# Kernel tuning notes

Measured on AMD Instinct MI355X. Metric: run time of the kernel, lower is better.

The kernel has to match this reference:

```python
import jax, jax.numpy as jnp
import numpy as np

N_MELS, HIDDEN, HEAD_DIM = 80, 128, 64


def _gru_step(h, gx_t, w_hh, b_hh):
    # PyTorch GRU cell math. gx_t = x_t @ W_ih^T + b_ih, precomputed. [B, 3H]
    H = h.shape[-1]
    gh = h @ w_hh.T + b_hh  # [B, 3H]
    r = jax.nn.sigmoid(gx_t[:, :H] + gh[:, :H])
    z = jax.nn.sigmoid(gx_t[:, H:2 * H] + gh[:, H:2 * H])
    n = jnp.tanh(gx_t[:, 2 * H:] + r * gh[:, 2 * H:])
    return (1.0 - z) * n + z * h


def setup_inputs() -> dict:
    key = jax.random.key(0)
    ks = jax.random.split(key, 14)
    s = 1.0 / np.sqrt(HIDDEN)
    u = lambda k, shape, sc: jax.random.uniform(k, shape, jnp.float32, -sc, sc)
    return {
        "x": jax.random.normal(ks[0], (128, 1500, N_MELS), dtype=jnp.float32),
        # forward-direction GRU params
        "w_ih_f": u(ks[1], (3 * HIDDEN, N_MELS), s),
        "w_hh_f": u(ks[2], (3 * HIDDEN, HIDDEN), s),
        "b_ih_f": u(ks[3], (3 * HIDDEN,), s),
        "b_hh_f": u(ks[4], (3 * HIDDEN,), s),
        # backward-direction GRU params
        "w_ih_b": u(ks[5], (3 * HIDDEN, N_MELS), s),
        "w_hh_b": u(ks[6], (3 * HIDDEN, HIDDEN), s),
        "b_ih_b": u(ks[7], (3 * HIDDEN,), s),
        "b_hh_b": u(ks[8], (3 * HIDDEN,), s),
        # MLP head: Linear(2H, 64) -> ReLU -> Linear(64, 1)
        "w1": u(ks[9], (HEAD_DIM, 2 * HIDDEN), 1.0 / np.sqrt(2 * HIDDEN)),
        "b1": u(ks[10], (HEAD_DIM,), 1.0 / np.sqrt(2 * HIDDEN)),
        "w2": u(ks[11], (1, HEAD_DIM), 1.0 / np.sqrt(HEAD_DIM)),
        "b2": u(ks[12], (1,), 1.0 / np.sqrt(HEAD_DIM)),
    }


def reference(x, w_ih_f, w_hh_f, b_ih_f, b_hh_f, w_ih_b, w_hh_b, b_ih_b, b_hh_b, w1, b1, w2, b2):
    B, T, _ = x.shape
    h0 = jnp.zeros((B, HIDDEN), dtype=x.dtype)

    # Forward direction: last output = final hidden state after full scan.
    # Precompute input projections for all timesteps in one GEMM.
    gx_f = jnp.einsum('bti,gi->tbg', x, w_ih_f) + b_ih_f  # [T, B, 3H]
    h_f, _ = jax.lax.scan(lambda h, g: (_gru_step(h, g, w_hh_f, b_hh_f), None), h0, gx_f)

    # Backward direction: out[:, -1, H:] in PyTorch is the backward hidden
    # after processing ONLY x[:, -1] (the reverse scan's first step), so a
    # single GRU step from h0 reproduces it exactly.
    gx_b_last = x[:, -1, :] @ w_ih_b.T + b_ih_b  # [B, 3H]
    h_b = _gru_step(h0, gx_b_last, w_hh_b, b_hh_b)

    last = jnp.concatenate([h_f, h_b], axis=-1)  # [B, 2H]
    # Head (eval mode: dropout is identity)
    hdn = jax.nn.relu(last @ w1.T + b1)
    out = hdn @ w2.T + b2  # [B, 1]
    return out[:, 0]
```

## Files before the change

### kernel.cpp

```cpp
#include <hip/hip_runtime.h>

#define B 128
#define T 1500
#define NI 80
#define H 128
#define G 384
#define TT 64

typedef float v2f __attribute__((ext_vector_type(2)));

__device__ __forceinline__ float sigf(float x) { return 1.0f / (1.0f + __expf(-x)); }
__device__ __forceinline__ float tanhfast(float x) { return 1.0f - 2.0f / (1.0f + __expf(2.0f * x)); }
__device__ __forceinline__ v2f pkfma(v2f a, v2f b, v2f c) { return __builtin_elementwise_fma(a, b, c); }

__global__ __launch_bounds__(384)
void gx_gemm_kernel(const float* __restrict__ x, const float* __restrict__ w_ih,
                    const float* __restrict__ b_ih, float* __restrict__ gx,
                    int t0, int ct) {
    int tile = blockIdx.x;
    int b = blockIdx.y;
    int tl0 = tile * TT;
    if (tl0 >= ct) return;
    int n = (ct - tl0 < TT) ? (ct - tl0) : TT;
    int tid = threadIdx.x;

    __shared__ __align__(16) float xs[TT * NI];
    const float4* xsrc4 = (const float4*)(x + ((size_t)b * T + (size_t)(t0 + tl0)) * NI);
    int total4 = n * (NI / 4);
    for (int i = tid; i < total4; i += 384) ((float4*)xs)[i] = xsrc4[i];

    v2f w2[40];
    const v2f* wr = (const v2f*)(w_ih + (size_t)tid * NI);
#pragma unroll
    for (int i = 0; i < 40; ++i) w2[i] = wr[i];
    float bias = b_ih[tid];
    __syncthreads();

    float* gout = gx + ((size_t)b * ct + (size_t)tl0) * G + tid;
    int tt = 0;
    for (; tt + 2 <= n; tt += 2) {
        const float4* xa4 = (const float4*)(xs + tt * NI);
        const float4* xb4 = (const float4*)(xs + (tt + 1) * NI);
        v2f a0 = {0.f, 0.f}, a1 = {0.f, 0.f}, c0 = {0.f, 0.f}, c1 = {0.f, 0.f};
#pragma unroll
        for (int i = 0; i < 20; ++i) {
            float4 xa = xa4[i];
            float4 xb = xb4[i];
            v2f alo = {xa.x, xa.y}, ahi = {xa.z, xa.w};
            v2f blo = {xb.x, xb.y}, bhi = {xb.z, xb.w};
            a0 = pkfma(w2[2 * i], alo, a0);
            a1 = pkfma(w2[2 * i + 1], ahi, a1);
            c0 = pkfma(w2[2 * i], blo, c0);
            c1 = pkfma(w2[2 * i + 1], bhi, c1);
        }
        gout[(size_t)tt * G]       = bias + ((a0.x + a0.y) + (a1.x + a1.y));
        gout[(size_t)(tt + 1) * G] = bias + ((c0.x + c0.y) + (c1.x + c1.y));
    }
    if (tt < n) {
        const float4* xa4 = (const float4*)(xs + tt * NI);
        v2f a0 = {0.f, 0.f}, a1 = {0.f, 0.f};
#pragma unroll
        for (int i = 0; i < 20; ++i) {
            float4 xa = xa4[i];
            v2f alo = {xa.x, xa.y}, ahi = {xa.z, xa.w};
            a0 = pkfma(w2[2 * i], alo, a0);
            a1 = pkfma(w2[2 * i + 1], ahi, a1);
        }
        gout[(size_t)tt * G] = bias + ((a0.x + a0.y) + (a1.x + a1.y));
    }
}

__global__ __launch_bounds__(512)
void scan_kernel(const float* __restrict__ gx, const float* __restrict__ w_hh,
                 const float* __restrict__ b_hh, float* __restrict__ h_state,
                 int ct, int first, int last,
                 const float* __restrict__ x,
                 const float* __restrict__ w_ih_b, const float* __restrict__ b_ih_b,
                 const float* __restrict__ b_hh_b,
                 const float* __restrict__ w1, const float* __restrict__ b1,
                 const float* __restrict__ w2, const float* __restrict__ b2,
                 float* __restrict__ out) {
    int b = blockIdx.x;
    int tid = threadIdx.x;
    int j = tid >> 2;
    int q = tid & 3;
    int jpad = j + ((j >> 5) << 2);

    __shared__ __align__(16) float hs0[144];
    __shared__ __align__(16) float hs1[144];
    __shared__ __align__(16) float tail_gx[G];
    __shared__ __align__(16) float last_s[2 * H];
    __shared__ __align__(16) float xb_s[NI];

    v2f WR[16], WZ[16], WN[16];
    {
        const v2f* p0 = (const v2f*)(w_hh + (size_t)j * H + 32 * q);
        const v2f* p1 = (const v2f*)(w_hh + (size_t)(j + H) * H + 32 * q);
        const v2f* p2 = (const v2f*)(w_hh + (size_t)(j + 2 * H) * H + 32 * q);
#pragma unroll
        for (int i = 0; i < 16; ++i) { WR[i] = p0[i]; WZ[i] = p1[i]; WN[i] = p2[i]; }
    }
    float br = b_hh[j], bz = b_hh[j + H], bn = b_hh[j + 2 * H];

    float h_cur = 0.f;
    if (!first) h_cur = h_state[b * H + j];
    if (q == 0) hs0[jpad] = h_cur;

    float ga0, ga1, ga2, gb0 = 0.f, gb1 = 0.f, gb2 = 0.f;
    {
        const float* gp = gx + (size_t)b * ct * G;
        ga0 = gp[j]; ga1 = gp[j + H]; ga2 = gp[j + 2 * H];
        if (ct > 1) { gb0 = gp[G + j]; gb1 = gp[G + j + H]; gb2 = gp[G + j + 2 * H]; }
    }
    asm volatile("s_waitcnt lgkmcnt(0)\n\ts_barrier" ::: "memory");

    auto step = [&](int TL, const float* SRC, float* DST, float& g0, float& g1, float& g2) {
        const float4* hv4 = (const float4*)(SRC + 36 * q);
        v2f arv = {0.f, 0.f}, azv = {0.f, 0.f}, anv = {0.f, 0.f};
#pragma unroll
        for (int i = 0; i < 8; ++i) {
            float4 hv = hv4[i];
            v2f hlo = {hv.x, hv.y}, hhi = {hv.z, hv.w};
            arv = pkfma(WR[2 * i], hlo, arv);
            azv = pkfma(WZ[2 * i], hlo, azv);
            anv = pkfma(WN[2 * i], hlo, anv);
            arv = pkfma(WR[2 * i + 1], hhi, arv);
            azv = pkfma(WZ[2 * i + 1], hhi, azv);
            anv = pkfma(WN[2 * i + 1], hhi, anv);
        }
        float ar = arv.x + arv.y, az = azv.x + azv.y, an = anv.x + anv.y;
        ar += __shfl_xor(ar, 1); az += __shfl_xor(az, 1); an += __shfl_xor(an, 1);
        ar += __shfl_xor(ar, 2); az += __shfl_xor(az, 2); an += __shfl_xor(an, 2);
        float r = sigf(g0 + br + ar);
        float z = sigf(g1 + bz + az);
        float n = tanhfast(g2 + r * (bn + an));
        h_cur = (1.f - z) * n + z * h_cur;
        if (q == 0) DST[jpad] = h_cur;
        if (TL + 2 < ct) {
            const float* gp = gx + ((size_t)b * ct + TL + 2) * G;
            g0 = gp[j]; g1 = gp[j + H]; g2 = gp[j + 2 * H];
        }
        asm volatile("s_waitcnt lgkmcnt(0)\n\ts_barrier" ::: "memory");
    };

    int tl = 0;
    for (; tl + 1 < ct; tl += 2) {
        step(tl,     hs0, hs1, ga0, ga1, ga2);
        step(tl + 1, hs1, hs0, gb0, gb1, gb2);
    }
    if (tl < ct) step(tl, hs0, hs1, ga0, ga1, ga2);

    if (!last) {
        if (q == 0) h_state[b * H + j] = h_cur;
        return;
    }

    if (tid < NI) xb_s[tid] = x[((size_t)b * T + (T - 1)) * NI + tid];
    if (q == 0) last_s[j] = h_cur;
    __syncthreads();

    if (tid < G) {
        const float4* wbr = (const float4*)(w_ih_b + (size_t)tid * NI);
        const float4* xv = (const float4*)xb_s;
        float a0 = 0.f, a1 = 0.f, a2 = 0.f, a3 = 0.f;
#pragma unroll
        for (int i = 0; i < 20; ++i) {
            float4 wv = wbr[i]; float4 x4 = xv[i];
            a0 = fmaf(wv.x, x4.x, a0); a1 = fmaf(wv.y, x4.y, a1);
            a2 = fmaf(wv.z, x4.z, a2); a3 = fmaf(wv.w, x4.w, a3);
        }
        tail_gx[tid] = b_ih_b[tid] + ((a0 + a1) + (a2 + a3));
    }
    __syncthreads();

    if (tid < H) {
        float r = sigf(tail_gx[tid] + b_hh_b[tid]);
        float z = sigf(tail_gx[tid + H] + b_hh_b[tid + H]);
        float n = tanhfast(tail_gx[tid + 2 * H] + r * b_hh_b[tid + 2 * H]);
        last_s[H + tid] = (1.f - z) * n;
    }
    __syncthreads();

    if (tid < 64) {
        const float4* w1r = (const float4*)(w1 + (size_t)tid * 2 * H);
        const float4* lv = (const float4*)last_s;
        float a0 = 0.f, a1 = 0.f, a2 = 0.f, a3 = 0.f;
#pragma unroll
        for (int i = 0; i < 64; ++i) {
            float4 wv = w1r[i]; float4 l4 = lv[i];
            a0 = fmaf(wv.x, l4.x, a0); a1 = fmaf(wv.y, l4.y, a1);
            a2 = fmaf(wv.z, l4.z, a2); a3 = fmaf(wv.w, l4.w, a3);
        }
        float v = b1[tid] + ((a0 + a1) + (a2 + a3));
        v = fmaxf(v, 0.f) * w2[tid];
#pragma unroll
        for (int off = 32; off > 0; off >>= 1) v += __shfl_down(v, off);
        if (tid == 0) out[b] = v + b2[0];
    }
}

extern "C" void kernel_launch(void* const* d_in, const int* in_sizes, int n_in,
                              void* d_out, int out_size, void* d_ws, size_t ws_size,
                              hipStream_t stream) {
    (void)in_sizes; (void)n_in; (void)out_size;
    const float* x      = (const float*)d_in[0];
    const float* w_ih_f = (const float*)d_in[1];
    const float* w_hh_f = (const float*)d_in[2];
    const float* b_ih_f = (const float*)d_in[3];
    const float* b_hh_f = (const float*)d_in[4];
    const float* w_ih_b = (const float*)d_in[5];
    const float* w_hh_b = (const float*)d_in[6];
    const float* b_ih_b = (const float*)d_in[7];
    const float* b_hh_b = (const float*)d_in[8];
    const float* w1     = (const float*)d_in[9];
    const float* b1     = (const float*)d_in[10];
    const float* w2     = (const float*)d_in[11];
    const float* b2     = (const float*)d_in[12];
    (void)w_hh_b;
    float* out = (float*)d_out;

    float* h_state = (float*)d_ws;
    float* gxbuf = h_state + B * H;
    size_t hbytes = (size_t)B * H * sizeof(float);
    size_t avail = ws_size > hbytes ? ws_size - hbytes : 0;
    long long chunkT = (long long)(avail / ((size_t)B * G * sizeof(float)));
    if (chunkT > T) chunkT = T;
    if (chunkT < 1) chunkT = 1;

    for (int t0 = 0; t0 < T; t0 += (int)chunkT) {
        int ct = (T - t0 < (int)chunkT) ? (T - t0) : (int)chunkT;
        int ntiles = (ct + TT - 1) / TT;
        gx_gemm_kernel<<<dim3(ntiles, B), dim3(384), 0, stream>>>(
            x, w_ih_f, b_ih_f, gxbuf, t0, ct);
        scan_kernel<<<dim3(B), dim3(512), 0, stream>>>(
            gxbuf, w_hh_f, b_hh_f, h_state, ct,
            (t0 == 0) ? 1 : 0, (t0 + ct >= T) ? 1 : 0,
            x, w_ih_b, b_ih_b, b_hh_b, w1, b1, w2, b2, out);
    }
}
```

Measured before the change: 1.163 ms.

## Fuse input projection into the GRU scan kernel, dropping the gx buffer

```diff
diff --git a/kernel.cpp b/kernel.cpp
--- a/kernel.cpp
+++ b/kernel.cpp
@@ -5,7 +5,6 @@
 #define NI 80
 #define H 128
 #define G 384
-#define TT 64
 
 typedef float v2f __attribute__((ext_vector_type(2)));
 
@@ -13,73 +12,15 @@
 __device__ __forceinline__ float tanhfast(float x) { return 1.0f - 2.0f / (1.0f + __expf(2.0f * x)); }
 __device__ __forceinline__ v2f pkfma(v2f a, v2f b, v2f c) { return __builtin_elementwise_fma(a, b, c); }
 
-__global__ __launch_bounds__(384)
-void gx_gemm_kernel(const float* __restrict__ x, const float* __restrict__ w_ih,
-                    const float* __restrict__ b_ih, float* __restrict__ gx,
-                    int t0, int ct) {
-    int tile = blockIdx.x;
-    int b = blockIdx.y;
-    int tl0 = tile * TT;
-    if (tl0 >= ct) return;
-    int n = (ct - tl0 < TT) ? (ct - tl0) : TT;
-    int tid = threadIdx.x;
-
-    __shared__ __align__(16) float xs[TT * NI];
-    const float4* xsrc4 = (const float4*)(x + ((size_t)b * T + (size_t)(t0 + tl0)) * NI);
-    int total4 = n * (NI / 4);
-    for (int i = tid; i < total4; i += 384) ((float4*)xs)[i] = xsrc4[i];
-
-    v2f w2[40];
-    const v2f* wr = (const v2f*)(w_ih + (size_t)tid * NI);
-#pragma unroll
-    for (int i = 0; i < 40; ++i) w2[i] = wr[i];
-    float bias = b_ih[tid];
-    __syncthreads();
-
-    float* gout = gx + ((size_t)b * ct + (size_t)tl0) * G + tid;
-    int tt = 0;
-    for (; tt + 2 <= n; tt += 2) {
-        const float4* xa4 = (const float4*)(xs + tt * NI);
-        const float4* xb4 = (const float4*)(xs + (tt + 1) * NI);
-        v2f a0 = {0.f, 0.f}, a1 = {0.f, 0.f}, c0 = {0.f, 0.f}, c1 = {0.f, 0.f};
-#pragma unroll
-        for (int i = 0; i < 20; ++i) {
-            float4 xa = xa4[i];
-            float4 xb = xb4[i];
-            v2f alo = {xa.x, xa.y}, ahi = {xa.z, xa.w};
-            v2f blo = {xb.x, xb.y}, bhi = {xb.z, xb.w};
-            a0 = pkfma(w2[2 * i], alo, a0);
-            a1 = pkfma(w2[2 * i + 1], ahi, a1);
-            c0 = pkfma(w2[2 * i], blo, c0);
-            c1 = pkfma(w2[2 * i + 1], bhi, c1);
-        }
-        gout[(size_t)tt * G]       = bias + ((a0.x + a0.y) + (a1.x + a1.y));
-        gout[(size_t)(tt + 1) * G] = bias + ((c0.x + c0.y) + (c1.x + c1.y));
-    }
-    if (tt < n) {
-        const float4* xa4 = (const float4*)(xs + tt * NI);
-        v2f a0 = {0.f, 0.f}, a1 = {0.f, 0.f};
-#pragma unroll
-        for (int i = 0; i < 20; ++i) {
-            float4 xa = xa4[i];
-            v2f alo = {xa.x, xa.y}, ahi = {xa.z, xa.w};
-            a0 = pkfma(w2[2 * i], alo, a0);
-            a1 = pkfma(w2[2 * i + 1], ahi, a1);
-        }
-        gout[(size_t)tt * G] = bias + ((a0.x + a0.y) + (a1.x + a1.y));
-    }
-}
-
 __global__ __launch_bounds__(512)
-void scan_kernel(const float* __restrict__ gx, const float* __restrict__ w_hh,
-                 const float* __restrict__ b_hh, float* __restrict__ h_state,
-                 int ct, int first, int last,
-                 const float* __restrict__ x,
-                 const float* __restrict__ w_ih_b, const float* __restrict__ b_ih_b,
-                 const float* __restrict__ b_hh_b,
-                 const float* __restrict__ w1, const float* __restrict__ b1,
-                 const float* __restrict__ w2, const float* __restrict__ b2,
-                 float* __restrict__ out) {
+void fused_gru_kernel(const float* __restrict__ x,
+                      const float* __restrict__ w_ih, const float* __restrict__ b_ih,
+                      const float* __restrict__ w_hh, const float* __restrict__ b_hh,
+                      const float* __restrict__ w_ih_b, const float* __restrict__ b_ih_b,
+                      const float* __restrict__ b_hh_b,
+                      const float* __restrict__ w1, const float* __restrict__ b1,
+                      const float* __restrict__ w2, const float* __restrict__ b2,
+                      float* __restrict__ out) {
     int b = blockIdx.x;
     int tid = threadIdx.x;
     int j = tid >> 2;
@@ -100,59 +41,80 @@
 #pragma unroll
         for (int i = 0; i < 16; ++i) { WR[i] = p0[i]; WZ[i] = p1[i]; WN[i] = p2[i]; }
     }
-    float br = b_hh[j], bz = b_hh[j + H], bn = b_hh[j + 2 * H];
+    float4 XWR[5], XWZ[5], XWN[5];
+    {
+        const float4* p0 = (const float4*)(w_ih + (size_t)j * NI + 20 * q);
+        const float4* p1 = (const float4*)(w_ih + (size_t)(j + H) * NI + 20 * q);
+        const float4* p2 = (const float4*)(w_ih + (size_t)(j + 2 * H) * NI + 20 * q);
+#pragma unroll
+        for (int i = 0; i < 5; ++i) { XWR[i] = p0[i]; XWZ[i] = p1[i]; XWN[i] = p2[i]; }
+    }
+    float brz = b_hh[j] ;
+    float bzz = b_hh[j + H];
+    float bnh = b_hh[j + 2 * H];
+    float cr = b_ih[j] + brz;
+    float cz = b_ih[j + H] + bzz;
+    float cn = b_ih[j + 2 * H];
+
+    const float* xbase = x + (size_t)b * T * NI + 20 * q;
+    float4 XA[5], XB[5];
+#pragma unroll
+    for (int i = 0; i < 5; ++i) XA[i] = *(const float4*)(xbase + i * 4);
+#pragma unroll
+    for (int i = 0; i < 5; ++i) XB[i] = *(const float4*)(xbase + NI + i * 4);
 
     float h_cur = 0.f;
-    if (!first) h_cur = h_state[b * H + j];
-    if (q == 0) hs0[jpad] = h_cur;
+    if (q == 0) hs0[jpad] = 0.f;
+    __syncthreads();
 
-    float ga0, ga1, ga2, gb0 = 0.f, gb1 = 0.f, gb2 = 0.f;
-    {
-        const float* gp = gx + (size_t)b * ct * G;
-        ga0 = gp[j]; ga1 = gp[j + H]; ga2 = gp[j + 2 * H];
-        if (ct > 1) { gb0 = gp[G + j]; gb1 = gp[G + j + H]; gb2 = gp[G + j + 2 * H]; }
-    }
-    asm volatile("s_waitcnt lgkmcnt(0)\n\ts_barrier" ::: "memory");
-
-    auto step = [&](int TL, const float* SRC, float* DST, float& g0, float& g1, float& g2) {
+    auto step = [&](int TL, const float* SRC, float* DST, float4 (&XC)[5]) {
         const float4* hv4 = (const float4*)(SRC + 36 * q);
-        v2f arv = {0.f, 0.f}, azv = {0.f, 0.f}, anv = {0.f, 0.f};
+        v2f arv = {0.f, 0.f}, azv = {0.f, 0.f}, anh = {0.f, 0.f}, anx = {0.f, 0.f};
 #pragma unroll
         for (int i = 0; i < 8; ++i) {
             float4 hv = hv4[i];
             v2f hlo = {hv.x, hv.y}, hhi = {hv.z, hv.w};
             arv = pkfma(WR[2 * i], hlo, arv);
             azv = pkfma(WZ[2 * i], hlo, azv);
-            anv = pkfma(WN[2 * i], hlo, anv);
+            anh = pkfma(WN[2 * i], hlo, anh);
             arv = pkfma(WR[2 * i + 1], hhi, arv);
             azv = pkfma(WZ[2 * i + 1], hhi, azv);
-            anv = pkfma(WN[2 * i + 1], hhi, anv);
+            anh = pkfma(WN[2 * i + 1], hhi, anh);
         }
-        float ar = arv.x + arv.y, az = azv.x + azv.y, an = anv.x + anv.y;
-        ar += __shfl_xor(ar, 1); az += __shfl_xor(az, 1); an += __shfl_xor(an, 1);
-        ar += __shfl_xor(ar, 2); az += __shfl_xor(az, 2); an += __shfl_xor(an, 2);
-        float r = sigf(g0 + br + ar);
-        float z = sigf(g1 + bz + az);
-        float n = tanhfast(g2 + r * (bn + an));
+#pragma unroll
+        for (int i = 0; i < 5; ++i) {
+            float4 xv = XC[i];
+            v2f xlo = {xv.x, xv.y}, xhi = {xv.z, xv.w};
+            arv = pkfma(v2f{XWR[i].x, XWR[i].y}, xlo, arv);
+            azv = pkfma(v2f{XWZ[i].x, XWZ[i].y}, xlo, azv);
+            anx = pkfma(v2f{XWN[i].x, XWN[i].y}, xlo, anx);
+            arv = pkfma(v2f{XWR[i].z, XWR[i].w}, xhi, arv);
+            azv = pkfma(v2f{XWZ[i].z, XWZ[i].w}, xhi, azv);
+            anx = pkfma(v2f{XWN[i].z, XWN[i].w}, xhi, anx);
+        }
+        {
+            int rt = TL + 2 < T ? TL + 2 : T - 1;
+            const float* xp = xbase + (size_t)rt * NI;
+#pragma unroll
+            for (int i = 0; i < 5; ++i) XC[i] = *(const float4*)(xp + i * 4);
+        }
+        float ar = arv.x + arv.y, az = azv.x + azv.y;
+        float ah = anh.x + anh.y, ax = anx.x + anx.y;
+        ar += __shfl_xor(ar, 1); az += __shfl_xor(az, 1);
+        ah += __shfl_xor(ah, 1); ax += __shfl_xor(ax, 1);
+        ar += __shfl_xor(ar, 2); az += __shfl_xor(az, 2);
+        ah += __shfl_xor(ah, 2); ax += __shfl_xor(ax, 2);
+        float r = sigf(cr + ar);
+        float z = sigf(cz + az);
+        float n = tanhfast((cn + ax) + r * (bnh + ah));
         h_cur = (1.f - z) * n + z * h_cur;
         if (q == 0) DST[jpad] = h_cur;
-        if (TL + 2 < ct) {
-            const float* gp = gx + ((size_t)b * ct + TL + 2) * G;
-            g0 = gp[j]; g1 = gp[j + H]; g2 = gp[j + 2 * H];
-        }
         asm volatile("s_waitcnt lgkmcnt(0)\n\ts_barrier" ::: "memory");
     };
 
-    int tl = 0;
-    for (; tl + 1 < ct; tl += 2) {
-        step(tl,     hs0, hs1, ga0, ga1, ga2);
-        step(tl + 1, hs1, hs0, gb0, gb1, gb2);
-    }
-    if (tl < ct) step(tl, hs0, hs1, ga0, ga1, ga2);
-
-    if (!last) {
-        if (q == 0) h_state[b * H + j] = h_cur;
-        return;
+    for (int tl = 0; tl < T; tl += 2) {
+        step(tl,     hs0, hs1, XA);
+        step(tl + 1, hs1, hs0, XB);
     }
 
     if (tid < NI) xb_s[tid] = x[((size_t)b * T + (T - 1)) * NI + tid];
@@ -202,7 +164,7 @@
 extern "C" void kernel_launch(void* const* d_in, const int* in_sizes, int n_in,
                               void* d_out, int out_size, void* d_ws, size_t ws_size,
                               hipStream_t stream) {
-    (void)in_sizes; (void)n_in; (void)out_size;
+    (void)in_sizes; (void)n_in; (void)out_size; (void)d_ws; (void)ws_size;
     const float* x      = (const float*)d_in[0];
     const float* w_ih_f = (const float*)d_in[1];
     const float* w_hh_f = (const float*)d_in[2];
@@ -219,22 +181,7 @@
     (void)w_hh_b;
     float* out = (float*)d_out;
 
-    float* h_state = (float*)d_ws;
-    float* gxbuf = h_state + B * H;
-    size_t hbytes = (size_t)B * H * sizeof(float);
-    size_t avail = ws_size > hbytes ? ws_size - hbytes : 0;
-    long long chunkT = (long long)(avail / ((size_t)B * G * sizeof(float)));
-    if (chunkT > T) chunkT = T;
-    if (chunkT < 1) chunkT = 1;
-
-    for (int t0 = 0; t0 < T; t0 += (int)chunkT) {
-        int ct = (T - t0 < (int)chunkT) ? (T - t0) : (int)chunkT;
-        int ntiles = (ct + TT - 1) / TT;
-        gx_gemm_kernel<<<dim3(ntiles, B), dim3(384), 0, stream>>>(
-            x, w_ih_f, b_ih_f, gxbuf, t0, ct);
-        scan_kernel<<<dim3(B), dim3(512), 0, stream>>>(
-            gxbuf, w_hh_f, b_hh_f, h_state, ct,
-            (t0 == 0) ? 1 : 0, (t0 + ct >= T) ? 1 : 0,
-            x, w_ih_b, b_ih_b, b_hh_b, w1, b1, w2, b2, out);
-    }
+    fused_gru_kernel<<<dim3(B), dim3(512), 0, stream>>>(
+        x, w_ih_f, b_ih_f, w_hh_f, b_hh_f,
+        w_ih_b, b_ih_b, b_hh_b, w1, b1, w2, b2, out);
 }
```

After: 1.250 ms. 7.4% more time.

## Stage gx tiles in double-buffered LDS and use DPP quad reductions

Applied to the files above, without the earlier changes.

```diff
diff --git a/kernel.cpp b/kernel.cpp
--- a/kernel.cpp
+++ b/kernel.cpp
@@ -6,12 +6,22 @@
 #define H 128
 #define G 384
 #define TT 64
+#define TS 16
 
 typedef float v2f __attribute__((ext_vector_type(2)));
 
 __device__ __forceinline__ float sigf(float x) { return 1.0f / (1.0f + __expf(-x)); }
 __device__ __forceinline__ float tanhfast(float x) { return 1.0f - 2.0f / (1.0f + __expf(2.0f * x)); }
 __device__ __forceinline__ v2f pkfma(v2f a, v2f b, v2f c) { return __builtin_elementwise_fma(a, b, c); }
+
+__device__ __forceinline__ float qsum(float v) {
+    int a = __builtin_bit_cast(int, v);
+    int b = __builtin_amdgcn_update_dpp(0, a, 0xB1, 0xF, 0xF, true);
+    float s = v + __builtin_bit_cast(float, b);
+    int c = __builtin_bit_cast(int, s);
+    int d = __builtin_amdgcn_update_dpp(0, c, 0x4E, 0xF, 0xF, true);
+    return s + __builtin_bit_cast(float, d);
+}
 
 __global__ __launch_bounds__(384)
 void gx_gemm_kernel(const float* __restrict__ x, const float* __restrict__ w_ih,
@@ -88,6 +98,7 @@
 
     __shared__ __align__(16) float hs0[144];
     __shared__ __align__(16) float hs1[144];
+    __shared__ __align__(16) float gxs[2][TS * G];
     __shared__ __align__(16) float tail_gx[G];
     __shared__ __align__(16) float last_s[2 * H];
     __shared__ __align__(16) float xb_s[NI];
@@ -102,53 +113,80 @@
     }
     float br = b_hh[j], bz = b_hh[j + H], bn = b_hh[j + 2 * H];
 
+    const float4* gsrc4 = (const float4*)(gx + (size_t)b * ct * G);
+    size_t limit4 = (size_t)ct * (G / 4) - 1;
+    float4 gr[3];
+#pragma unroll
+    for (int i = 0; i < 3; ++i) {
+        size_t idx = (size_t)i * 512 + tid; if (idx > limit4) idx = limit4;
+        gr[i] = gsrc4[idx];
+    }
+    {
+        float4* d4 = (float4*)gxs[0];
+#pragma unroll
+        for (int i = 0; i < 3; ++i) d4[(size_t)i * 512 + tid] = gr[i];
+    }
+#pragma unroll
+    for (int i = 0; i < 3; ++i) {
+        size_t idx = (size_t)(TS * G / 4) + (size_t)i * 512 + tid; if (idx > limit4) idx = limit4;
+        gr[i] = gsrc4[idx];
+    }
+
     float h_cur = 0.f;
     if (!first) h_cur = h_state[b * H + j];
     if (q == 0) hs0[jpad] = h_cur;
-
-    float ga0, ga1, ga2, gb0 = 0.f, gb1 = 0.f, gb2 = 0.f;
-    {
-        const float* gp = gx + (size_t)b * ct * G;
-        ga0 = gp[j]; ga1 = gp[j + H]; ga2 = gp[j + 2 * H];
-        if (ct > 1) { gb0 = gp[G + j]; gb1 = gp[G + j + H]; gb2 = gp[G + j + 2 * H]; }
-    }
-    asm volatile("s_waitcnt lgkmcnt(0)\n\ts_barrier" ::: "memory");
-
-    auto step = [&](int TL, const float* SRC, float* DST, float& g0, float& g1, float& g2) {
-        const float4* hv4 = (const float4*)(SRC + 36 * q);
-        v2f arv = {0.f, 0.f}, azv = {0.f, 0.f}, anv = {0.f, 0.f};
-#pragma unroll
-        for (int i = 0; i < 8; ++i) {
-            float4 hv = hv4[i];
-            v2f hlo = {hv.x, hv.y}, hhi = {hv.z, hv.w};
-            arv = pkfma(WR[2 * i], hlo, arv);
-            azv = pkfma(WZ[2 * i], hlo, azv);
-            anv = pkfma(WN[2 * i], hlo, anv);
-            arv = pkfma(WR[2 * i + 1], hhi, arv);
-            azv = pkfma(WZ[2 * i + 1], hhi, azv);
-            anv = pkfma(WN[2 * i + 1], hhi, anv);
-        }
-        float ar = arv.x + arv.y, az = azv.x + azv.y, an = anv.x + anv.y;
-        ar += __shfl_xor(ar, 1); az += __shfl_xor(az, 1); an += __shfl_xor(an, 1);
-        ar += __shfl_xor(ar, 2); az += __shfl_xor(az, 2); an += __shfl_xor(an, 2);
-        float r = sigf(g0 + br + ar);
-        float z = sigf(g1 + bz + az);
-        float n = tanhfast(g2 + r * (bn + an));
-        h_cur = (1.f - z) * n + z * h_cur;
-        if (q == 0) DST[jpad] = h_cur;
-        if (TL + 2 < ct) {
-            const float* gp = gx + ((size_t)b * ct + TL + 2) * G;
-            g0 = gp[j]; g1 = gp[j + H]; g2 = gp[j + 2 * H];
-        }
-        asm volatile("s_waitcnt lgkmcnt(0)\n\ts_barrier" ::: "memory");
-    };
-
-    int tl = 0;
-    for (; tl + 1 < ct; tl += 2) {
-        step(tl,     hs0, hs1, ga0, ga1, ga2);
-        step(tl + 1, hs1, hs0, gb0, gb1, gb2);
-    }
-    if (tl < ct) step(tl, hs0, hs1, ga0, ga1, ga2);
+    __syncthreads();
+
+    float* hsrc = hs0;
+    float* hdst = hs1;
+    int ntiles = (ct + TS - 1) / TS;
+
+    for (int c = 0; c < ntiles; ++c) {
+        int ns = (ct - c * TS < TS) ? (ct - c * TS) : TS;
+        const float* gtile = gxs[c & 1];
+        for (int s = 0; s < ns; ++s) {
+            float g0 = gtile[s * G + j];
+            float g1 = gtile[s * G + j + H];
+            float g2 = gtile[s * G + j + 2 * H];
+            const float4* hv4 = (const float4*)(hsrc + 36 * q);
+            v2f arv = {0.f, 0.f}, azv = {0.f, 0.f}, anv = {0.f, 0.f};
+#pragma unroll
+            for (int i = 0; i < 8; ++i) {
+                float4 hv = hv4[i];
+                v2f hlo = {hv.x, hv.y}, hhi = {hv.z, hv.w};
+                arv = pkfma(WR[2 * i], hlo, arv);
+                azv = pkfma(WZ[2 * i], hlo, azv);
+                anv = pkfma(WN[2 * i], hlo, anv);
+                arv = pkfma(WR[2 * i + 1], hhi, arv);
+                azv = pkfma(WZ[2 * i + 1], hhi, azv);
+                anv = pkfma(WN[2 * i + 1], hhi, anv);
+            }
+            float ar = qsum(arv.x + arv.y);
+            float az = qsum(azv.x + azv.y);
+            float an = qsum(anv.x + anv.y);
+            float r = sigf(g0 + br + ar);
+            float z = sigf(g1 + bz + az);
+            float n = tanhfast(g2 + r * (bn + an));
+            h_cur = (1.f - z) * n + z * h_cur;
+            if (q == 0) hdst[jpad] = h_cur;
+            float* tmp = hsrc; hsrc = hdst; hdst = tmp;
+            asm volatile("s_waitcnt lgkmcnt(0)\n\ts_barrier" ::: "memory");
+        }
+        if (c + 1 < ntiles) {
+            float4* d4 = (float4*)gxs[(c + 1) & 1];
+#pragma unroll
+            for (int i = 0; i < 3; ++i) d4[(size_t)i * 512 + tid] = gr[i];
+            if (c + 2 < ntiles) {
+#pragma unroll
+                for (int i = 0; i < 3; ++i) {
+                    size_t idx = (size_t)(c + 2) * (TS * G / 4) + (size_t)i * 512 + tid;
+                    if (idx > limit4) idx = limit4;
+                    gr[i] = gsrc4[idx];
+                }
+            }
+            asm volatile("s_waitcnt lgkmcnt(0)\n\ts_barrier" ::: "memory");
+        }
+    }
 
     if (!last) {
         if (q == 0) h_state[b * H + j] = h_cur;
```

Result: slower. 1.316 ms (+13.2%).

## Pack two batch rows per scan block with 2-way k-split and DPP reduction

Applied to the files above, without the earlier changes.

```diff
diff --git a/kernel.cpp b/kernel.cpp
--- a/kernel.cpp
+++ b/kernel.cpp
@@ -12,6 +12,12 @@
 __device__ __forceinline__ float sigf(float x) { return 1.0f / (1.0f + __expf(-x)); }
 __device__ __forceinline__ float tanhfast(float x) { return 1.0f - 2.0f / (1.0f + __expf(2.0f * x)); }
 __device__ __forceinline__ v2f pkfma(v2f a, v2f b, v2f c) { return __builtin_elementwise_fma(a, b, c); }
+
+__device__ __forceinline__ float qsum1(float v) {
+    int a = __builtin_bit_cast(int, v);
+    int c = __builtin_amdgcn_update_dpp(0, a, 0xB1, 0xF, 0xF, true);
+    return v + __builtin_bit_cast(float, c);
+}
 
 __global__ __launch_bounds__(384)
 void gx_gemm_kernel(const float* __restrict__ x, const float* __restrict__ w_ih,
@@ -70,7 +76,7 @@
     }
 }
 
-__global__ __launch_bounds__(512)
+__global__ __launch_bounds__(512, 2)
 void scan_kernel(const float* __restrict__ gx, const float* __restrict__ w_hh,
                  const float* __restrict__ b_hh, float* __restrict__ h_state,
                  int ct, int first, int last,
@@ -80,31 +86,35 @@
                  const float* __restrict__ w1, const float* __restrict__ b1,
                  const float* __restrict__ w2, const float* __restrict__ b2,
                  float* __restrict__ out) {
-    int b = blockIdx.x;
     int tid = threadIdx.x;
-    int j = tid >> 2;
-    int q = tid & 3;
-    int jpad = j + ((j >> 5) << 2);
-
-    __shared__ __align__(16) float hs0[144];
-    __shared__ __align__(16) float hs1[144];
-    __shared__ __align__(16) float tail_gx[G];
-    __shared__ __align__(16) float last_s[2 * H];
-    __shared__ __align__(16) float xb_s[NI];
-
-    v2f WR[16], WZ[16], WN[16];
+    int half = tid >> 8;
+    int b = blockIdx.x * 2 + half;
+    int local = tid & 255;
+    int j = local >> 1;
+    int q = local & 1;
+    int jpad = j + ((j >> 6) << 2);
+
+    __shared__ __align__(16) float hs[2][2][132];
+    __shared__ __align__(16) float tail_gx[2][G];
+    __shared__ __align__(16) float last_s[2][2 * H];
+    __shared__ __align__(16) float xb_s[2][NI];
+
+    float4 WR4[16], WZ4[16], WN4[16];
     {
-        const v2f* p0 = (const v2f*)(w_hh + (size_t)j * H + 32 * q);
-        const v2f* p1 = (const v2f*)(w_hh + (size_t)(j + H) * H + 32 * q);
-        const v2f* p2 = (const v2f*)(w_hh + (size_t)(j + 2 * H) * H + 32 * q);
-#pragma unroll
-        for (int i = 0; i < 16; ++i) { WR[i] = p0[i]; WZ[i] = p1[i]; WN[i] = p2[i]; }
+        const float4* wp = (const float4*)w_hh;
+        size_t base = (size_t)j * 32 + 16 * q;
+#pragma unroll
+        for (int i = 0; i < 16; ++i) {
+            WR4[i] = wp[base + i];
+            WZ4[i] = wp[base + (size_t)H * 32 + i];
+            WN4[i] = wp[base + (size_t)2 * H * 32 + i];
+        }
     }
     float br = b_hh[j], bz = b_hh[j + H], bn = b_hh[j + 2 * H];
 
     float h_cur = 0.f;
     if (!first) h_cur = h_state[b * H + j];
-    if (q == 0) hs0[jpad] = h_cur;
+    if (q == 0) hs[half][0][jpad] = h_cur;
 
     float ga0, ga1, ga2, gb0 = 0.f, gb1 = 0.f, gb2 = 0.f;
     {
@@ -112,30 +122,33 @@
         ga0 = gp[j]; ga1 = gp[j + H]; ga2 = gp[j + 2 * H];
         if (ct > 1) { gb0 = gp[G + j]; gb1 = gp[G + j + H]; gb2 = gp[G + j + 2 * H]; }
     }
-    asm volatile("s_waitcnt lgkmcnt(0)\n\ts_barrier" ::: "memory");
-
-    auto step = [&](int TL, const float* SRC, float* DST, float& g0, float& g1, float& g2) {
-        const float4* hv4 = (const float4*)(SRC + 36 * q);
-        v2f arv = {0.f, 0.f}, azv = {0.f, 0.f}, anv = {0.f, 0.f};
-#pragma unroll
-        for (int i = 0; i < 8; ++i) {
+    __syncthreads();
+
+    auto step = [&](int TL, int SB, float& g0, float& g1, float& g2) {
+        const float4* hv4 = (const float4*)(&hs[half][SB][0] + 68 * q);
+        v2f arL = {0.f, 0.f}, arH = {0.f, 0.f};
+        v2f azL = {0.f, 0.f}, azH = {0.f, 0.f};
+        v2f anL = {0.f, 0.f}, anH = {0.f, 0.f};
+#pragma unroll
+        for (int i = 0; i < 16; ++i) {
             float4 hv = hv4[i];
             v2f hlo = {hv.x, hv.y}, hhi = {hv.z, hv.w};
-            arv = pkfma(WR[2 * i], hlo, arv);
-            azv = pkfma(WZ[2 * i], hlo, azv);
-            anv = pkfma(WN[2 * i], hlo, anv);
-            arv = pkfma(WR[2 * i + 1], hhi, arv);
-            azv = pkfma(WZ[2 * i + 1], hhi, azv);
-            anv = pkfma(WN[2 * i + 1], hhi, anv);
-        }
-        float ar = arv.x + arv.y, az = azv.x + azv.y, an = anv.x + anv.y;
-        ar += __shfl_xor(ar, 1); az += __shfl_xor(az, 1); an += __shfl_xor(an, 1);
-        ar += __shfl_xor(ar, 2); az += __shfl_xor(az, 2); an += __shfl_xor(an, 2);
+            arL = pkfma(v2f{WR4[i].x, WR4[i].y}, hlo, arL);
+            azL = pkfma(v2f{WZ4[i].x, WZ4[i].y}, hlo, azL);
+            anL = pkfma(v2f{WN4[i].x, WN4[i].y}, hlo, anL);
+            arH = pkfma(v2f{WR4[i].z, WR4[i].w}, hhi, arH);
+            azH = pkfma(v2f{WZ4[i].z, WZ4[i].w}, hhi, azH);
+            anH = pkfma(v2f{WN4[i].z, WN4[i].w}, hhi, anH);
+        }
+        float ar = (arL.x + arL.y) + (arH.x + arH.y);
+        float az = (azL.x + azL.y) + (azH.x + azH.y);
+        float an = (anL.x + anL.y) + (anH.x + anH.y);
+        ar = qsum1(ar); az = qsum1(az); an = qsum1(an);
         float r = sigf(g0 + br + ar);
         float z = sigf(g1 + bz + az);
         float n = tanhfast(g2 + r * (bn + an));
         h_cur = (1.f - z) * n + z * h_cur;
-        if (q == 0) DST[jpad] = h_cur;
+        if (q == 0) hs[half][SB ^ 1][jpad] = h_cur;
         if (TL + 2 < ct) {
             const float* gp = gx + ((size_t)b * ct + TL + 2) * G;
             g0 = gp[j]; g1 = gp[j + H]; g2 = gp[j + 2 * H];
@@ -145,23 +158,23 @@
 
     int tl = 0;
     for (; tl + 1 < ct; tl += 2) {
-        step(tl,     hs0, hs1, ga0, ga1, ga2);
-        step(tl + 1, hs1, hs0, gb0, gb1, gb2);
-    }
-    if (tl < ct) step(tl, hs0, hs1, ga0, ga1, ga2);
+        step(tl,     0, ga0, ga1, ga2);
+        step(tl + 1, 1, gb0, gb1, gb2);
+    }
+    if (tl < ct) step(tl, 0, ga0, ga1, ga2);
 
     if (!last) {
         if (q == 0) h_state[b * H + j] = h_cur;
         return;
     }
 
-    if (tid < NI) xb_s[tid] = x[((size_t)b * T + (T - 1)) * NI + tid];
-    if (q == 0) last_s[j] = h_cur;
-    __syncthreads();
-
-    if (tid < G) {
-        const float4* wbr = (const float4*)(w_ih_b + (size_t)tid * NI);
-        const float4* xv = (const float4*)xb_s;
+    if (local < NI) xb_s[half][local] = x[((size_t)b * T + (T - 1)) * NI + local];
+    if (q == 0) last_s[half][j] = h_cur;
+    __syncthreads();
+
+    for (int gg = local; gg < G; gg += 256) {
+        const float4* wbr = (const float4*)(w_ih_b + (size_t)gg * NI);
+        const float4* xv = (const float4*)xb_s[half];
         float a0 = 0.f, a1 = 0.f, a2 = 0.f, a3 = 0.f;
 #pragma unroll
         for (int i = 0; i < 20; ++i) {
@@ -169,21 +182,21 @@
             a0 = fmaf(wv.x, x4.x, a0); a1 = fmaf(wv.y, x4.y, a1);
             a2 = fmaf(wv.z, x4.z, a2); a3 = fmaf(wv.w, x4.w, a3);
         }
-        tail_gx[tid] = b_ih_b[tid] + ((a0 + a1) + (a2 + a3));
-    }
-    __syncthreads();
-
-    if (tid < H) {
-        float r = sigf(tail_gx[tid] + b_hh_b[tid]);
-        float z = sigf(tail_gx[tid + H] + b_hh_b[tid + H]);
-        float n = tanhfast(tail_gx[tid + 2 * H] + r * b_hh_b[tid + 2 * H]);
-        last_s[H + tid] = (1.f - z) * n;
-    }
-    __syncthreads();
-
-    if (tid < 64) {
-        const float4* w1r = (const float4*)(w1 + (size_t)tid * 2 * H);
-        const float4* lv = (const float4*)last_s;
+        tail_gx[half][gg] = b_ih_b[gg] + ((a0 + a1) + (a2 + a3));
+    }
+    __syncthreads();
+
+    if (local < H) {
+        float r = sigf(tail_gx[half][local] + b_hh_b[local]);
+        float z = sigf(tail_gx[half][local + H] + b_hh_b[local + H]);
+        float n = tanhfast(tail_gx[half][local + 2 * H] + r * b_hh_b[local + 2 * H]);
+        last_s[half][H + local] = (1.f - z) * n;
+    }
+    __syncthreads();
+
+    if (local < 64) {
+        const float4* w1r = (const float4*)(w1 + (size_t)local * 2 * H);
+        const float4* lv = (const float4*)last_s[half];
         float a0 = 0.f, a1 = 0.f, a2 = 0.f, a3 = 0.f;
 #pragma unroll
         for (int i = 0; i < 64; ++i) {
@@ -191,11 +204,11 @@
             a0 = fmaf(wv.x, l4.x, a0); a1 = fmaf(wv.y, l4.y, a1);
             a2 = fmaf(wv.z, l4.z, a2); a3 = fmaf(wv.w, l4.w, a3);
         }
-        float v = b1[tid] + ((a0 + a1) + (a2 + a3));
-        v = fmaxf(v, 0.f) * w2[tid];
+        float v = b1[local] + ((a0 + a1) + (a2 + a3));
+        v = fmaxf(v, 0.f) * w2[local];
 #pragma unroll
         for (int off = 32; off > 0; off >>= 1) v += __shfl_down(v, off);
-        if (tid == 0) out[b] = v + b2[0];
+        if (local == 0) out[b] = v + b2[0];
     }
 }
 
@@ -232,7 +245,7 @@
         int ntiles = (ct + TT - 1) / TT;
         gx_gemm_kernel<<<dim3(ntiles, B), dim3(384), 0, stream>>>(
             x, w_ih_f, b_ih_f, gxbuf, t0, ct);
-        scan_kernel<<<dim3(B), dim3(512), 0, stream>>>(
+        scan_kernel<<<dim3(B / 2), dim3(512), 0, stream>>>(
             gxbuf, w_hh_f, b_hh_f, h_state, ct,
             (t0 == 0) ? 1 : 0, (t0 + ct >= T) ? 1 : 0,
             x, w_ih_b, b_ih_b, b_hh_b, w1, b1, w2, b2, out);
```

Result: slower. 1.445 ms (+24.2%).
